# Kernel tuning notes

Hardware: AMD Instinct MI355X
Metric: run time of the kernel (lower is better)

## Reference

```python
import jax, jax.numpy as jnp
import numpy as np

B, S, V, D, P, H = 64, 512, 30522, 768, 8, 4
DH = D // H            # per-head dim = 192
NPER = 1 + P           # 1 text node + P concept nodes per example
N = B * NPER           # 576 total GNN nodes
E = 4096               # raw edges (before symmetrization)
EPS = 1e-6
NEG_SLOPE = 0.2


def gat_layer(x, src_i, dst_i, W, a_s, a_d, b):
    """Standard multi-head GAT layer (concat heads), edge-list formulation."""
    n = x.shape[0]
    h = (x @ W).reshape(n, H, DH)                      # [N,H,DH]
    alpha_s = jnp.einsum('nhd,hd->nh', h, a_s)          # [N,H]
    alpha_d = jnp.einsum('nhd,hd->nh', h, a_d)
    e = jax.nn.leaky_relu(alpha_s[src_i] + alpha_d[dst_i], NEG_SLOPE)  # [E,H]
    m = jax.ops.segment_max(e, dst_i, num_segments=n)   # stable softmax per dst
    ex = jnp.exp(e - m[dst_i])
    den = jax.ops.segment_sum(ex, dst_i, num_segments=n)
    att = ex / den[dst_i]                               # [E,H]
    msg = att[:, :, None] * h[src_i]                    # [E,H,DH]
    out = jax.ops.segment_sum(msg, dst_i, num_segments=n)
    return out.reshape(n, D) + b


def setup_inputs() -> dict:
    key = jax.random.key(0)
    ks = jax.random.split(key, 14)
    src = jax.random.randint(ks[0], (B, S), 0, V)
    seg = jax.random.randint(ks[1], (B, S), 0, 3)
    type_ids = jax.random.randint(ks[2], (B, S), 0, 21)
    pos = jnp.broadcast_to(jnp.arange(S, dtype=jnp.int64 if jax.config.jax_enable_x64 else jnp.int32), (B, S))
    span_start = jax.random.randint(ks[3], (B, P), 0, S - 8)
    span_len = jax.random.randint(ks[4], (B, P), 1, 8)
    span_end = span_start + span_len                    # end >= start, < S
    edge_idx = jax.random.randint(ks[5], (2, E), 0, N)
    word_table = jax.random.normal(ks[6], (V, D), dtype=jnp.float32) * 0.02
    pos_table = jax.random.normal(ks[7], (S, D), dtype=jnp.float32) * 0.02
    seg_table = jax.random.normal(ks[8], (3, D), dtype=jnp.float32) * 0.02
    type_table = jax.random.normal(ks[9], (21, D), dtype=jnp.float32) * 0.02
    gamma = jnp.ones((D,), jnp.float32)
    beta = jnp.zeros((D,), jnp.float32)
    W_gat = jax.random.normal(ks[10], (5, D, D), dtype=jnp.float32) * 0.05
    a_src = jax.random.normal(ks[11], (5, H, DH), dtype=jnp.float32) * 0.05
    a_dst = jax.random.normal(ks[12], (5, H, DH), dtype=jnp.float32) * 0.05
    b_gat = jnp.zeros((5, D), jnp.float32)
    return dict(src=src, seg=seg, type_ids=type_ids, pos=pos,
                span_start=span_start, span_end=span_end, edge_idx=edge_idx,
                word_table=word_table, pos_table=pos_table, seg_table=seg_table,
                type_table=type_table, gamma=gamma, beta=beta,
                W_gat=W_gat, a_src=a_src, a_dst=a_dst, b_gat=b_gat)


def reference(src, seg, type_ids, pos, span_start, span_end, edge_idx,
              word_table, pos_table, seg_table, type_table, gamma, beta,
              W_gat, a_src, a_dst, b_gat):
    word_emb = word_table[src]                                  # [B,S,D]
    # --- GNN node assembly: node 0 = CLS emb, nodes 1..P = span sums ---
    pref = jnp.concatenate([jnp.zeros((B, 1, D), word_emb.dtype),
                            jnp.cumsum(word_emb, axis=1)], axis=1)  # [B,S+1,D]
    g = lambda idx: jnp.take_along_axis(pref, idx[:, :, None], axis=1)
    concept = g(span_end + 1) - g(span_start)                   # [B,P,D] inclusive span sums
    nodes = jnp.concatenate([word_emb[:, :1, :], concept], axis=1).reshape(N, D)
    # --- symmetrize edges (code concatenates flipped copy); add self-loops ---
    loop = jnp.arange(N)
    si = jnp.concatenate([edge_idx[0], edge_idx[1], loop])
    di = jnp.concatenate([edge_idx[1], edge_idx[0], loop])
    # --- 5 GAT layers with GELU (dropout = identity at eval) ---
    x = nodes
    for l in range(5):
        x = jax.nn.gelu(gat_layer(x, si, di, W_gat[l], a_src[l], a_dst[l], b_gat[l]),
                        approximate=False)
    text_idx = jnp.arange(B) * NPER
    word_emb = word_emb.at[:, 0, :].set(x[text_idx])            # scatter back into CLS slot
    # --- sum of 4 embeddings + LayerNorm ---
    emb = word_emb + pos_table[pos] + seg_table[seg] + type_table[type_ids]
    mu = jnp.mean(emb, axis=-1, keepdims=True)
    var = jnp.mean((emb - mu) ** 2, axis=-1, keepdims=True)
    return gamma * (emb - mu) / jnp.sqrt(var + EPS) + beta
```

## Files before the change

kernel.cpp:

```cpp
#include <hip/hip_runtime.h>


#define DEV __device__ __forceinline__

typedef short s16x8 __attribute__((ext_vector_type(8)));
typedef float f32x4 __attribute__((ext_vector_type(4)));
typedef unsigned short u16x8 __attribute__((ext_vector_type(8)));

DEV float b2f(unsigned int u) { union { unsigned int i; float f; } v; v.i = u << 16; return v.f; }
DEV unsigned short f2b(float f) {
  union { float f; unsigned int i; } v; v.f = f;
  return (unsigned short)((v.i + 0x7fffu + ((v.i >> 16) & 1u)) >> 16);
}
DEV float gelu_exact(float x) { return 0.5f * x * (1.f + erff(x * 0.70710678118654752f)); }

DEV float ldf(const void* p, size_t i, int fF) {
  return fF ? ((const float*)p)[i] : b2f(((const unsigned short*)p)[i]);
}
DEV int ldi(const void* p, size_t i, int fI) {
  return fI ? ((const int*)p)[2 * i] : ((const int*)p)[i];
}

DEV size_t frag_off(int n, int d) {
  return ((((size_t)(n >> 4) * 24 + (size_t)(d >> 5)) * 64 +
           (((d >> 3) & 3) << 4) + (n & 15)) << 3) + (d & 7);
}

__global__ __launch_bounds__(256) void k_front(const void* __restrict__ src,
                                               const void* __restrict__ sst,
                                               const void* __restrict__ sen,
                                               const void* __restrict__ edge,
                                               const void* __restrict__ word,
                                               const void* __restrict__ pos,
                                               const void* __restrict__ aS,
                                               const void* __restrict__ aD,
                                               const void* __restrict__ Wg,
                                               unsigned short* __restrict__ xh,
                                               unsigned short* __restrict__ xl,
                                               unsigned short* __restrict__ Bh,
                                               unsigned short* __restrict__ Bl,
                                               int* __restrict__ csr_off,
                                               int* __restrict__ csr_src,
                                               int* __restrict__ flags) {
  __shared__ int sflags[2];
  __shared__ float tile[64][65];
  __shared__ float sA[768], sD[768];
  __shared__ int cnt[576], off[577], fill[576];
  int t = threadIdx.x, bid = blockIdx.x;
  if (t < 64) {
    const unsigned short* w16 = (const unsigned short*)word;
    int crazy = 0;
    for (int i = t; i < 512; i += 64) {
      unsigned int e = (w16[i] >> 7) & 0xffu;
      if (e >= 135u || (e >= 1u && e <= 100u)) crazy++;
    }
#pragma unroll
    for (int o = 32; o > 0; o >>= 1) crazy += __shfl_down(crazy, o);
    if (t == 0) {
      sflags[0] = (crazy >= 8) ? 1 : 0;
      sflags[1] = (((const int*)pos)[1] == 0) ? 1 : 0;
    }
  }
  __syncthreads();
  int fF = sflags[0], fI = sflags[1];
  if (bid == 0 && t == 0) { flags[0] = fF; flags[1] = fI; }

  if (bid < 780) {
    int layer = bid / 156, r = bid % 156, kt = r / 13, nt = r % 13;
    int k0 = kt * 64, n0 = nt * 64;
    if (nt < 12) {
      if (fF) {
        const float* Wf = (const float*)Wg;
#pragma unroll
        for (int i = 0; i < 4; ++i) {
          int e = t + 256 * i, rk = e >> 4, c4 = (e & 15) * 4;
          f32x4 v = *(const f32x4*)(Wf + ((size_t)layer * 768 + k0 + rk) * 768 + n0 + c4);
          tile[rk][c4] = v[0]; tile[rk][c4 + 1] = v[1];
          tile[rk][c4 + 2] = v[2]; tile[rk][c4 + 3] = v[3];
        }
      } else {
#pragma unroll
        for (int i = 0; i < 16; ++i) {
          int e = t + 256 * i, rk = e >> 6, cn = e & 63;
          tile[rk][cn] = ldf(Wg, ((size_t)layer * 768 + k0 + rk) * 768 + n0 + cn, fF);
        }
      }
    } else {
      for (int i = t; i < 768; i += 256) {
        sA[i] = ldf(aS, (size_t)layer * 768 + i, fF);
        sD[i] = ldf(aD, (size_t)layer * 768 + i, fF);
      }
#pragma unroll
      for (int i = 0; i < 16; ++i) {
        int e = t + 256 * i, rk = e >> 6, cn = e & 63;
        if (cn >= 8) tile[rk][cn] = 0.f;
      }
      __syncthreads();
      int wave = t >> 6, lane = t & 63;
      for (int rr = 0; rr < 16; ++rr) {
        int rk = wave * 16 + rr;
        size_t wbase = ((size_t)layer * 768 + k0 + rk) * 768;
        float accS[4] = {0.f, 0.f, 0.f, 0.f}, accD[4] = {0.f, 0.f, 0.f, 0.f};
#pragma unroll
        for (int i = 0; i < 12; ++i) {
          int d = lane + 64 * i;
          float w = ldf(Wg, wbase + d, fF);
          accS[i / 3] += w * sA[d];
          accD[i / 3] += w * sD[d];
        }
#pragma unroll
        for (int h = 0; h < 4; ++h) {
          float sS = accS[h], sDv = accD[h];
#pragma unroll
          for (int o = 32; o > 0; o >>= 1) {
            sS += __shfl_down(sS, o);
            sDv += __shfl_down(sDv, o);
          }
          if (lane == 0) { tile[rk][h] = sS; tile[rk][4 + h] = sDv; }
        }
      }
    }
    __syncthreads();
    size_t lb = (size_t)layer * 79872;
#pragma unroll
    for (int g = 0; g < 2; ++g) {
      int G = t * 2 + g, rn = G & 63, c8 = G >> 6;
      int n = n0 + rn, kb = k0 + c8 * 8;
      u16x8 hv, lv;
#pragma unroll
      for (int j = 0; j < 8; ++j) {
        float v = tile[c8 * 8 + j][rn];
        unsigned short hi = f2b(v);
        hv[j] = hi;
        lv[j] = f2b(v - b2f((unsigned int)hi));
      }
      size_t go = lb + ((size_t)(n >> 4) * 24 + (size_t)(kb >> 5)) * 64 +
                  (((kb >> 3) & 3) << 4) + (n & 15);
      *(u16x8*)(Bh + go * 8) = hv;
      *(u16x8*)(Bl + go * 8) = lv;
    }
  } else if (bid < 1356) {
    int g = bid - 780;
    int b = g / 9, j = g % 9;
    float v[3] = {0.f, 0.f, 0.f};
    if (j == 0) {
      int rr = ldi(src, (size_t)b * 512, fI);
#pragma unroll
      for (int ii = 0; ii < 3; ++ii) v[ii] = ldf(word, (size_t)rr * 768 + t + 256 * ii, fF);
    } else {
      int st = ldi(sst, (size_t)b * 8 + j - 1, fI);
      int en = ldi(sen, (size_t)b * 8 + j - 1, fI);
      int cntr = en - st + 1;
      int rows[8];
#pragma unroll 8
      for (int q = 0; q < 8; ++q)
        if (q < cntr) rows[q] = ldi(src, (size_t)b * 512 + st + q, fI);
      for (int q = 0; q < cntr; ++q) {
        int rr = rows[q];
#pragma unroll
        for (int ii = 0; ii < 3; ++ii) v[ii] += ldf(word, (size_t)rr * 768 + t + 256 * ii, fF);
      }
    }
#pragma unroll
    for (int ii = 0; ii < 3; ++ii) {
      int d = t + 256 * ii;
      unsigned short hi = f2b(v[ii]);
      size_t o = frag_off(g, d);
      xh[o] = hi;
      xl[o] = f2b(v[ii] - b2f((unsigned int)hi));
    }
  } else {
    for (int i = t; i < 576; i += 256) cnt[i] = 0;
    __syncthreads();
    for (int e = t; e < 8768; e += 256) {
      int di;
      if (e < 4096) di = ldi(edge, (size_t)4096 + e, fI);
      else if (e < 8192) di = ldi(edge, (size_t)e - 4096, fI);
      else di = e - 8192;
      atomicAdd(&cnt[di], 1);
    }
    __syncthreads();
    if (t == 0) {
      int a = 0;
      for (int i = 0; i < 576; ++i) { off[i] = a; a += cnt[i]; }
      off[576] = a;
    }
    __syncthreads();
    for (int i = t; i < 577; i += 256) csr_off[i] = off[i];
    for (int i = t; i < 576; i += 256) fill[i] = off[i];
    __syncthreads();
    for (int e = t; e < 8768; e += 256) {
      int si, di;
      if (e < 4096)      { si = ldi(edge, (size_t)e, fI); di = ldi(edge, (size_t)4096 + e, fI); }
      else if (e < 8192) { si = ldi(edge, (size_t)e, fI); di = ldi(edge, (size_t)e - 4096, fI); }
      else               { si = e - 8192;                 di = si; }
      int p = atomicAdd(&fill[di], 1);
      csr_src[p] = si;
    }
  }
}

__global__ __launch_bounds__(256) void k_gemm(const unsigned short* __restrict__ xh,
                                              const unsigned short* __restrict__ xl,
                                              const unsigned short* __restrict__ Bh,
                                              const unsigned short* __restrict__ Bl,
                                              float* __restrict__ C) {
  int t = threadIdx.x, wave = t >> 6, lane = t & 63;
  int bid = blockIdx.x;
  int xcd = bid & 7, slot = bid >> 3;
  int v = (xcd < 4) ? (xcd * 59 + slot) : (236 + (xcd - 4) * 58 + slot);
  int rtg = v % 18, ctg = v / 18;
  int rt = rtg * 2 + (wave >> 1), ct = ctg * 2 + (wave & 1);
  const s16x8* Ah = (const s16x8*)xh + (size_t)rt * 1536 + lane;
  const s16x8* Al = (const s16x8*)xl + (size_t)rt * 1536 + lane;
  const s16x8* Bhp = (const s16x8*)Bh + (size_t)ct * 1536 + lane;
  const s16x8* Blp = (const s16x8*)Bl + (size_t)ct * 1536 + lane;
  f32x4 a0 = {0.f, 0.f, 0.f, 0.f}, a1 = a0, a2 = a0;
#pragma unroll 6
  for (int kk = 0; kk < 24; ++kk) {
    s16x8 ah = Ah[kk * 64];
    s16x8 al = Al[kk * 64];
    s16x8 bh = Bhp[kk * 64];
    s16x8 bl = Blp[kk * 64];
    a0 = __builtin_amdgcn_mfma_f32_16x16x32_bf16(ah, bh, a0, 0, 0, 0);
    a1 = __builtin_amdgcn_mfma_f32_16x16x32_bf16(ah, bl, a1, 0, 0, 0);
    a2 = __builtin_amdgcn_mfma_f32_16x16x32_bf16(al, bh, a2, 0, 0, 0);
  }
  int row0 = rt * 16 + (lane >> 4) * 4, col = ct * 16 + (lane & 15);
#pragma unroll
  for (int r = 0; r < 4; ++r)
    C[(size_t)(row0 + r) * 832 + col] = a0[r] + a1[r] + a2[r];
}

DEV float gat_aggregate(const float* __restrict__ C, const int* __restrict__ off,
                        const int* __restrict__ srcs, int n, int d, int h) {
  float aDv = C[(size_t)n * 832 + 772 + h];
  int e0 = off[n], e1 = off[n + 1];
  float num = 0.f, den = 0.f;
  for (int e = e0; e < e1; e += 4) {
    float lg[4], ms[4];
#pragma unroll
    for (int j = 0; j < 4; ++j) {
      int ee = (e + j < e1) ? (e + j) : e0;
      int s = srcs[ee];
      lg[j] = C[(size_t)s * 832 + 768 + h];
      ms[j] = C[(size_t)s * 832 + d];
    }
#pragma unroll
    for (int j = 0; j < 4; ++j) {
      if (e + j < e1) {
        float l = lg[j] + aDv;
        float lrel = l < 0.f ? 0.2f * l : l;
        lrel = fminf(fmaxf(lrel, -60.f), 40.f);
        float w = __expf(lrel);
        num += w * ms[j];
        den += w;
      }
    }
  }
  return num / den;
}

__global__ __launch_bounds__(256) void k_gat(const float* __restrict__ C,
                                             const int* __restrict__ off,
                                             const int* __restrict__ srcs,
                                             const void* __restrict__ bG,
                                             const int* __restrict__ flg,
                                             int layer,
                                             unsigned short* __restrict__ xh,
                                             unsigned short* __restrict__ xl) {
  int fF = flg[0];
  int idx = blockIdx.x * 256 + threadIdx.x;
  int n = idx / 768, d = idx - n * 768, h = d / 192;
  float g = gelu_exact(gat_aggregate(C, off, srcs, n, d, h) +
                       ldf(bG, (size_t)layer * 768 + d, fF));
  unsigned short hi = f2b(g);
  size_t o = frag_off(n, d);
  xh[o] = hi;
  xl[o] = f2b(g - b2f((unsigned int)hi));
}

__global__ __launch_bounds__(256) void k_gat_last(const float* __restrict__ C,
                                                  const int* __restrict__ off,
                                                  const int* __restrict__ srcs,
                                                  const void* __restrict__ bG,
                                                  const int* __restrict__ flg,
                                                  float* __restrict__ xf) {
  int fF = flg[0];
  int idx = blockIdx.x * 256 + threadIdx.x;
  int b = idx / 768, d = idx - b * 768, h = d / 192;
  int n = b * 9;
  float g = gelu_exact(gat_aggregate(C, off, srcs, n, d, h) +
                       ldf(bG, (size_t)4 * 768 + d, fF));
  xf[(size_t)n * 768 + d] = g;
}

DEV void final_row_f32(int r, int lane, const f32x4* wsrc,
                       const void* seg, const void* typ, const void* post,
                       const void* segt, const void* typt,
                       const void* gamma, const void* beta, int fI,
                       float* __restrict__ outp) {
  int s = r & 511;
  int sg = ldi(seg, (size_t)r, fI), tp = ldi(typ, (size_t)r, fI);
  const f32x4* pr = (const f32x4*)((const float*)post + (size_t)s * 768);
  const f32x4* sr = (const f32x4*)((const float*)segt + (size_t)sg * 768);
  const f32x4* tr = (const f32x4*)((const float*)typt + (size_t)tp * 768);
  float sum = 0.f, sq = 0.f;
  f32x4 vv[3];
#pragma unroll
  for (int j = 0; j < 3; ++j) {
    int p = lane + 64 * j;
    f32x4 a = wsrc[j];
    a += pr[p]; a += sr[p]; a += tr[p];
    vv[j] = a;
#pragma unroll
    for (int c = 0; c < 4; ++c) { sum += a[c]; sq += a[c] * a[c]; }
  }
#pragma unroll
  for (int o = 32; o > 0; o >>= 1) { sum += __shfl_down(sum, o); sq += __shfl_down(sq, o); }
  sum = __shfl(sum, 0); sq = __shfl(sq, 0);
  float mu = sum * (1.f / 768.f);
  float var = fmaxf(sq * (1.f / 768.f) - mu * mu, 0.f);
  float rstd = rsqrtf(var + 1e-6f);
  const f32x4* gm = (const f32x4*)gamma;
  const f32x4* bt = (const f32x4*)beta;
  f32x4* orow = (f32x4*)(outp + (size_t)r * 768);
#pragma unroll
  for (int j = 0; j < 3; ++j) {
    int p = lane + 64 * j;
    f32x4 g4 = gm[p], b4 = bt[p], y;
#pragma unroll
    for (int c = 0; c < 4; ++c) y[c] = g4[c] * (vv[j][c] - mu) * rstd + b4[c];
    __builtin_nontemporal_store(y, &orow[p]);
  }
}

DEV void final_row_bf16(int r, int lane, const void* src, const void* seg,
                        const void* typ, const void* word, const void* post,
                        const void* segt, const void* typt, const void* gamma,
                        const void* beta, const float* xf, int fI,
                        unsigned short* __restrict__ outp) {
  int b = r >> 9, s = r & 511;
  int sg = ldi(seg, (size_t)r, fI), tp = ldi(typ, (size_t)r, fI);
  int wrow = ldi(src, (size_t)r, fI);
  bool cls = (s == 0);
  float sum = 0.f, sq = 0.f;
  float vs[12];
#pragma unroll
  for (int j = 0; j < 12; ++j) {
    int d = lane + 64 * j;
    float xv = cls ? xf[(size_t)b * 6912 + d] : ldf(word, (size_t)wrow * 768 + d, 0);
    xv += ldf(post, (size_t)s * 768 + d, 0);
    xv += ldf(segt, (size_t)sg * 768 + d, 0);
    xv += ldf(typt, (size_t)tp * 768 + d, 0);
    vs[j] = xv;
    sum += xv; sq += xv * xv;
  }
#pragma unroll
  for (int o = 32; o > 0; o >>= 1) { sum += __shfl_down(sum, o); sq += __shfl_down(sq, o); }
  sum = __shfl(sum, 0); sq = __shfl(sq, 0);
  float mu = sum * (1.f / 768.f);
  float var = fmaxf(sq * (1.f / 768.f) - mu * mu, 0.f);
  float rstd = rsqrtf(var + 1e-6f);
#pragma unroll
  for (int j = 0; j < 12; ++j) {
    int d = lane + 64 * j;
    float y = ldf(gamma, (size_t)d, 0) * (vs[j] - mu) * rstd + ldf(beta, (size_t)d, 0);
    outp[(size_t)r * 768 + d] = f2b(y);
  }
}

__global__ __launch_bounds__(256) void k_final(const void* __restrict__ src,
                                               const void* __restrict__ seg,
                                               const void* __restrict__ typ,
                                               const void* __restrict__ word,
                                               const void* __restrict__ post,
                                               const void* __restrict__ segt,
                                               const void* __restrict__ typt,
                                               const void* __restrict__ gamma,
                                               const void* __restrict__ beta,
                                               const float* __restrict__ xf,
                                               const int* __restrict__ flg,
                                               void* __restrict__ out) {
  int fF = flg[0], fI = flg[1];
  int wave = threadIdx.x >> 6, lane = threadIdx.x & 63;
  int r0 = blockIdx.x * 4 + wave, r1 = r0 + 16384;
  if (fF) {
    int s0 = r0 & 511, s1 = r1 & 511;
    int b0 = r0 >> 9, b1 = r1 >> 9;
    int w0r = ldi(src, (size_t)r0, fI), w1r = ldi(src, (size_t)r1, fI);
    const f32x4* p0 = (s0 == 0) ? (const f32x4*)(xf + (size_t)b0 * 6912)
                                : (const f32x4*)((const float*)word + (size_t)w0r * 768);
    const f32x4* p1 = (s1 == 0) ? (const f32x4*)(xf + (size_t)b1 * 6912)
                                : (const f32x4*)((const float*)word + (size_t)w1r * 768);
    f32x4 wa[3], wb[3];
#pragma unroll
    for (int j = 0; j < 3; ++j) { wa[j] = p0[lane + 64 * j]; wb[j] = p1[lane + 64 * j]; }
    final_row_f32(r0, lane, wa, seg, typ, post, segt, typt, gamma, beta, fI, (float*)out);
    final_row_f32(r1, lane, wb, seg, typ, post, segt, typt, gamma, beta, fI, (float*)out);
  } else {
    final_row_bf16(r0, lane, src, seg, typ, word, post, segt, typt, gamma, beta, xf, fI,
                   (unsigned short*)out);
    final_row_bf16(r1, lane, src, seg, typ, word, post, segt, typt, gamma, beta, xf, fI,
                   (unsigned short*)out);
  }
}

extern "C" void kernel_launch(void* const* d_in, const int* in_sizes, int n_in,
                              void* d_out, int out_size, void* d_ws, size_t ws_size,
                              hipStream_t stream) {
  const void* src  = d_in[0];
  const void* seg  = d_in[1];
  const void* typ  = d_in[2];
  const void* pos  = d_in[3];
  const void* sst  = d_in[4];
  const void* sen  = d_in[5];
  const void* edge = d_in[6];
  const void* word = d_in[7];
  const void* post = d_in[8];
  const void* segt = d_in[9];
  const void* typt = d_in[10];
  const void* gamma = d_in[11];
  const void* beta  = d_in[12];
  const void* Wg    = d_in[13];
  const void* aS    = d_in[14];
  const void* aD    = d_in[15];
  const void* bG    = d_in[16];

  char* ws = (char*)d_ws;
  float* xf = (float*)(ws);
  float* C  = (float*)(ws + 1769472);
  unsigned short* xh = (unsigned short*)(ws + 3686400);
  unsigned short* xl = (unsigned short*)(ws + 4571136);
  unsigned short* Bh = (unsigned short*)(ws + 5455872);
  unsigned short* Bl = (unsigned short*)(ws + 11845632);
  int* csr_off = (int*)(ws + 18358272);
  int* csr_src = (int*)(ws + 18360592);
  int* flags   = (int*)(ws + 18395664);

  k_front<<<dim3(1357), dim3(256), 0, stream>>>(src, sst, sen, edge, word, pos, aS, aD, Wg,
                                                xh, xl, Bh, Bl, csr_off, csr_src, flags);
  for (int l = 0; l < 4; ++l) {
    k_gemm<<<dim3(468), dim3(256), 0, stream>>>(xh, xl,
                                                Bh + (size_t)l * 832 * 768,
                                                Bl + (size_t)l * 832 * 768, C);
    k_gat<<<dim3(1728), dim3(256), 0, stream>>>(C, csr_off, csr_src, bG, flags, l, xh, xl);
  }
  k_gemm<<<dim3(468), dim3(256), 0, stream>>>(xh, xl,
                                              Bh + (size_t)4 * 832 * 768,
                                              Bl + (size_t)4 * 832 * 768, C);
  k_gat_last<<<dim3(192), dim3(256), 0, stream>>>(C, csr_off, csr_src, bG, flags, xf);
  k_final<<<dim3(4096), dim3(256), 0, stream>>>(src, seg, typ, word, post, segt, typt,
                                                gamma, beta, xf, flags, d_out);
}
```

Baseline: 369.8 us.

## Fuse last GAT aggregation into final LayerNorm kernel and simplify GEMM tile mapping

Removes the separate k_gat_last launch. The CLS rows inside k_final now compute the last-layer GAT aggregation and GELU directly from C. The GEMM block-to-tile mapping also switches from an XCD-aware swizzle to a plain linear wave-to-tile mapping. This saves one kernel launch and the xf round trip. In exchange, only the few waves holding CLS rows do a long serial aggregation, and L2 locality in the GEMM may suffer.

```diff
diff --git a/kernel.cpp b/kernel.cpp
--- a/kernel.cpp
+++ b/kernel.cpp
@@ -205,12 +205,9 @@
                                               const unsigned short* __restrict__ Bh,
                                               const unsigned short* __restrict__ Bl,
                                               float* __restrict__ C) {
-  int t = threadIdx.x, wave = t >> 6, lane = t & 63;
-  int bid = blockIdx.x;
-  int xcd = bid & 7, slot = bid >> 3;
-  int v = (xcd < 4) ? (xcd * 59 + slot) : (236 + (xcd - 4) * 58 + slot);
-  int rtg = v % 18, ctg = v / 18;
-  int rt = rtg * 2 + (wave >> 1), ct = ctg * 2 + (wave & 1);
+  int t = threadIdx.x;
+  int wid = blockIdx.x * 4 + (t >> 6), lane = t & 63;
+  int rt = wid / 52, ct = wid % 52;
   const s16x8* Ah = (const s16x8*)xh + (size_t)rt * 1536 + lane;
   const s16x8* Al = (const s16x8*)xl + (size_t)rt * 1536 + lane;
   const s16x8* Bhp = (const s16x8*)Bh + (size_t)ct * 1536 + lane;
@@ -280,21 +277,6 @@
   xl[o] = f2b(g - b2f((unsigned int)hi));
 }
 
-__global__ __launch_bounds__(256) void k_gat_last(const float* __restrict__ C,
-                                                  const int* __restrict__ off,
-                                                  const int* __restrict__ srcs,
-                                                  const void* __restrict__ bG,
-                                                  const int* __restrict__ flg,
-                                                  float* __restrict__ xf) {
-  int fF = flg[0];
-  int idx = blockIdx.x * 256 + threadIdx.x;
-  int b = idx / 768, d = idx - b * 768, h = d / 192;
-  int n = b * 9;
-  float g = gelu_exact(gat_aggregate(C, off, srcs, n, d, h) +
-                       ldf(bG, (size_t)4 * 768 + d, fF));
-  xf[(size_t)n * 768 + d] = g;
-}
-
 DEV void final_row_f32(int r, int lane, const f32x4* wsrc,
                        const void* seg, const void* typ, const void* post,
                        const void* segt, const void* typt,
@@ -338,7 +320,9 @@
 DEV void final_row_bf16(int r, int lane, const void* src, const void* seg,
                         const void* typ, const void* word, const void* post,
                         const void* segt, const void* typt, const void* gamma,
-                        const void* beta, const float* xf, int fI,
+                        const void* beta, const float* __restrict__ C,
+                        const int* __restrict__ off, const int* __restrict__ srcs,
+                        const void* bG, int fI,
                         unsigned short* __restrict__ outp) {
   int b = r >> 9, s = r & 511;
   int sg = ldi(seg, (size_t)r, fI), tp = ldi(typ, (size_t)r, fI);
@@ -349,7 +333,13 @@
 #pragma unroll
   for (int j = 0; j < 12; ++j) {
     int d = lane + 64 * j;
-    float xv = cls ? xf[(size_t)b * 6912 + d] : ldf(word, (size_t)wrow * 768 + d, 0);
+    float xv;
+    if (cls) {
+      xv = gelu_exact(gat_aggregate(C, off, srcs, b * 9, d, d / 192) +
+                      ldf(bG, (size_t)4 * 768 + d, 0));
+    } else {
+      xv = ldf(word, (size_t)wrow * 768 + d, 0);
+    }
     xv += ldf(post, (size_t)s * 768 + d, 0);
     xv += ldf(segt, (size_t)sg * 768 + d, 0);
     xv += ldf(typt, (size_t)tp * 768 + d, 0);
@@ -367,6 +357,21 @@
     int d = lane + 64 * j;
     float y = ldf(gamma, (size_t)d, 0) * (vs[j] - mu) * rstd + ldf(beta, (size_t)d, 0);
     outp[(size_t)r * 768 + d] = f2b(y);
+  }
+}
+
+DEV void cls_fill_f32(const float* __restrict__ C, const int* __restrict__ off,
+                      const int* __restrict__ srcs, const void* bG, int fF,
+                      int b, int lane, f32x4* wa) {
+  int n = b * 9;
+#pragma unroll
+  for (int j = 0; j < 3; ++j) {
+#pragma unroll
+    for (int c = 0; c < 4; ++c) {
+      int d = (lane + 64 * j) * 4 + c;
+      wa[j][c] = gelu_exact(gat_aggregate(C, off, srcs, n, d, d / 192) +
+                            ldf(bG, (size_t)4 * 768 + d, fF));
+    }
   }
 }
 
@@ -379,7 +384,10 @@
                                                const void* __restrict__ typt,
                                                const void* __restrict__ gamma,
                                                const void* __restrict__ beta,
-                                               const float* __restrict__ xf,
+                                               const float* __restrict__ C,
+                                               const int* __restrict__ csr_off,
+                                               const int* __restrict__ csr_src,
+                                               const void* __restrict__ bG,
                                                const int* __restrict__ flg,
                                                void* __restrict__ out) {
   int fF = flg[0], fI = flg[1];
@@ -389,20 +397,33 @@
     int s0 = r0 & 511, s1 = r1 & 511;
     int b0 = r0 >> 9, b1 = r1 >> 9;
     int w0r = ldi(src, (size_t)r0, fI), w1r = ldi(src, (size_t)r1, fI);
-    const f32x4* p0 = (s0 == 0) ? (const f32x4*)(xf + (size_t)b0 * 6912)
-                                : (const f32x4*)((const float*)word + (size_t)w0r * 768);
-    const f32x4* p1 = (s1 == 0) ? (const f32x4*)(xf + (size_t)b1 * 6912)
-                                : (const f32x4*)((const float*)word + (size_t)w1r * 768);
     f32x4 wa[3], wb[3];
-#pragma unroll
-    for (int j = 0; j < 3; ++j) { wa[j] = p0[lane + 64 * j]; wb[j] = p1[lane + 64 * j]; }
+    if (s0 != 0 && s1 != 0) {
+      const f32x4* p0 = (const f32x4*)((const float*)word + (size_t)w0r * 768);
+      const f32x4* p1 = (const f32x4*)((const float*)word + (size_t)w1r * 768);
+#pragma unroll
+      for (int j = 0; j < 3; ++j) { wa[j] = p0[lane + 64 * j]; wb[j] = p1[lane + 64 * j]; }
+    } else {
+      if (s0 == 0) cls_fill_f32(C, csr_off, csr_src, bG, fF, b0, lane, wa);
+      else {
+        const f32x4* p0 = (const f32x4*)((const float*)word + (size_t)w0r * 768);
+#pragma unroll
+        for (int j = 0; j < 3; ++j) wa[j] = p0[lane + 64 * j];
+      }
+      if (s1 == 0) cls_fill_f32(C, csr_off, csr_src, bG, fF, b1, lane, wb);
+      else {
+        const f32x4* p1 = (const f32x4*)((const float*)word + (size_t)w1r * 768);
+#pragma unroll
+        for (int j = 0; j < 3; ++j) wb[j] = p1[lane + 64 * j];
+      }
+    }
     final_row_f32(r0, lane, wa, seg, typ, post, segt, typt, gamma, beta, fI, (float*)out);
     final_row_f32(r1, lane, wb, seg, typ, post, segt, typt, gamma, beta, fI, (float*)out);
   } else {
-    final_row_bf16(r0, lane, src, seg, typ, word, post, segt, typt, gamma, beta, xf, fI,
-                   (unsigned short*)out);
-    final_row_bf16(r1, lane, src, seg, typ, word, post, segt, typt, gamma, beta, xf, fI,
-                   (unsigned short*)out);
+    final_row_bf16(r0, lane, src, seg, typ, word, post, segt, typt, gamma, beta,
+                   C, csr_off, csr_src, bG, fI, (unsigned short*)out);
+    final_row_bf16(r1, lane, src, seg, typ, word, post, segt, typt, gamma, beta,
+                   C, csr_off, csr_src, bG, fI, (unsigned short*)out);
   }
 }
 
@@ -428,7 +449,6 @@
   const void* bG    = d_in[16];
 
   char* ws = (char*)d_ws;
-  float* xf = (float*)(ws);
   float* C  = (float*)(ws + 1769472);
   unsigned short* xh = (unsigned short*)(ws + 3686400);
   unsigned short* xl = (unsigned short*)(ws + 4571136);
@@ -449,7 +469,7 @@
   k_gemm<<<dim3(468), dim3(256), 0, stream>>>(xh, xl,
                                               Bh + (size_t)4 * 832 * 768,
                                               Bl + (size_t)4 * 832 * 768, C);
-  k_gat_last<<<dim3(192), dim3(256), 0, stream>>>(C, csr_off, csr_src, bG, flags, xf);
   k_final<<<dim3(4096), dim3(256), 0, stream>>>(src, seg, typ, word, post, segt, typt,
-                                                gamma, beta, xf, flags, d_out);
-}
+                                                gamma, beta, C, csr_off, csr_src, bG,
+                                                flags, d_out);
+}
```

Result: slower. 440.6 us (+19.1%).
